# Performance work log

Measured on AMD Instinct MI355X. Metric: run time of the kernel, lower is better.

The kernel has to match this reference:

```python
import math
import jax, jax.numpy as jnp
import numpy as np

N_HEAD = 8


def setup_inputs() -> dict:
    key = jax.random.key(0)
    ks = jax.random.split(key, 9)
    B, S, D = 4, 2048, 512
    s = 1.0 / math.sqrt(D)
    return {
        "x": jax.random.normal(ks[0], (B, S, D), jnp.float32),
        "Wq": jax.random.normal(ks[1], (D, D), jnp.float32) * s,
        "bq": jax.random.normal(ks[2], (D,), jnp.float32) * s,
        "Wk": jax.random.normal(ks[3], (D, D), jnp.float32) * s,
        "bk": jax.random.normal(ks[4], (D,), jnp.float32) * s,
        "Wv": jax.random.normal(ks[5], (D, D), jnp.float32) * s,
        "bv": jax.random.normal(ks[6], (D,), jnp.float32) * s,
        "Wo": jax.random.normal(ks[7], (D, D), jnp.float32) * s,
        "bo": jax.random.normal(ks[8], (D,), jnp.float32) * s,
    }


def reference(x, Wq, bq, Wk, bk, Wv, bv, Wo, bo):
    B, S, D = x.shape
    H = N_HEAD
    hd = D // H
    # projections -> [B, H, S, hd]
    def split_heads(y):
        return y.reshape(B, S, H, hd).transpose(0, 2, 1, 3)
    q = split_heads(x @ Wq + bq)
    k = split_heads(x @ Wk + bk)
    v = split_heads(x @ Wv + bv)
    scale = 1.0 / math.sqrt(hd)
    scores = jnp.einsum("bhqd,bhkd->bhqk", q, k) * scale  # [B,H,S,S]
    attn = jax.nn.softmax(scores, axis=-1)
    ctx = jnp.einsum("bhqk,bhkd->bhqd", attn, v)  # [B,H,S,hd]
    ctx = ctx.transpose(0, 2, 1, 3).reshape(B, S, D)
    out = ctx @ Wo + bo
    avg_attn = attn.mean(axis=1)  # [B,S,S]
    return out, avg_attn
```

## Files before the change

### kernel.cpp

```cpp
#include <hip/hip_runtime.h>

typedef __bf16 bf16;
typedef __bf16 bf16x8 __attribute__((ext_vector_type(8)));
typedef float  f32x4  __attribute__((ext_vector_type(4)));

#define MFMA16(a,b,c) __builtin_amdgcn_mfma_f32_16x16x32_bf16((a),(b),(c),0,0,0)

#define BATCH 4
#define SEQ   2048
#define DIM   512
#define NH    8
#define HD    64
#define QSCALE 0.18033688f

__device__ __forceinline__ bf16x8 ldsfrag(const bf16* t, int row, int kc, int quad){
    int unit = ((kc << 2) + quad) ^ (row & 7);
    return *(const bf16x8*)(t + row * 64 + unit * 8);
}

__device__ __forceinline__ void stage64x64(const bf16* src, long rowStride, bf16* dst, int tid){
#pragma unroll
    for (int rnd = 0; rnd < 2; ++rnd){
        int sid = tid + rnd * 256;
        int row = sid >> 3, s = sid & 7;
        bf16x8 val = *(const bf16x8*)(src + (long)row * rowStride + s * 8);
        *(bf16x8*)(dst + row * 64 + ((s ^ (row & 7)) << 3)) = val;
    }
}

__global__ __launch_bounds__(256) void cvt_x(const float* __restrict__ x, bf16* __restrict__ xb){
    int i = blockIdx.x * 256 + threadIdx.x;
    float4 f = ((const float4*)x)[i];
    bf16* o = xb + 4 * (long)i;
    o[0] = (bf16)f.x; o[1] = (bf16)f.y; o[2] = (bf16)f.z; o[3] = (bf16)f.w;
}

__global__ __launch_bounds__(256) void cvt_wt(const float* __restrict__ Wq, const float* __restrict__ Wk,
                                              const float* __restrict__ Wv, const float* __restrict__ Wo,
                                              bf16* __restrict__ WTb){
    int z = blockIdx.z;
    const float* W = (z == 0) ? Wq : (z == 1) ? Wk : (z == 2) ? Wv : Wo;
    bf16* WT = WTb + (long)z * DIM * DIM;
    __shared__ float lt[32 * 33];
    int t = threadIdx.x, r0 = t >> 5, c = t & 31;
    int k0 = blockIdx.x * 32, n0 = blockIdx.y * 32;
#pragma unroll
    for (int i = 0; i < 4; ++i){
        int row = r0 + i * 8;
        lt[row * 33 + c] = W[(long)(k0 + row) * DIM + n0 + c];
    }
    __syncthreads();
#pragma unroll
    for (int i = 0; i < 4; ++i){
        int nr = r0 + i * 8;
        WT[(long)(n0 + nr) * DIM + k0 + c] = (bf16)lt[c * 33 + nr];
    }
}

__global__ __launch_bounds__(256) void gemm_qkv(const bf16* __restrict__ X, const bf16* __restrict__ WTb,
                                                const float* __restrict__ bq, const float* __restrict__ bk,
                                                const float* __restrict__ bv, bf16* __restrict__ outb){
    __shared__ __align__(16) bf16 lA[128 * 64];
    __shared__ __align__(16) bf16 lB[128 * 64];
    int z = blockIdx.z;
    const bf16* WT = WTb + (long)z * DIM * DIM;
    const float* bias = (z == 0) ? bq : (z == 1) ? bk : bv;
    float qs = (z == 0) ? QSCALE : 1.0f;
    bf16* out = outb + (long)z * BATCH * SEQ * DIM;
    int tid = threadIdx.x, lane = tid & 63, w = tid >> 6;
    int wm = w >> 1, wn = w & 1;
    int m0 = blockIdx.y * 128, n0 = blockIdx.x * 128;
    int r16 = lane & 15, quad = lane >> 4;
    f32x4 zz = {0.f, 0.f, 0.f, 0.f};
    f32x4 acc[4][4];
#pragma unroll
    for (int a = 0; a < 4; ++a)
#pragma unroll
        for (int b2 = 0; b2 < 4; ++b2) acc[a][b2] = zz;

    for (int k0 = 0; k0 < DIM; k0 += 64){
        __syncthreads();
#pragma unroll
        for (int rnd = 0; rnd < 4; ++rnd){
            int sid = tid + rnd * 256;
            int row = sid >> 3, s = sid & 7;
            *(bf16x8*)(lA + row * 64 + ((s ^ (row & 7)) << 3)) =
                *(const bf16x8*)(X + (long)(m0 + row) * DIM + k0 + s * 8);
            *(bf16x8*)(lB + row * 64 + ((s ^ (row & 7)) << 3)) =
                *(const bf16x8*)(WT + (long)(n0 + row) * DIM + k0 + s * 8);
        }
        __syncthreads();
#pragma unroll
        for (int kc = 0; kc < 2; ++kc){
            bf16x8 aF[4], bF[4];
#pragma unroll
            for (int i = 0; i < 4; ++i){
                aF[i] = ldsfrag(lA, wm * 64 + i * 16 + r16, kc, quad);
                bF[i] = ldsfrag(lB, wn * 64 + i * 16 + r16, kc, quad);
            }
#pragma unroll
            for (int rb = 0; rb < 4; ++rb)
#pragma unroll
                for (int nb = 0; nb < 4; ++nb)
                    acc[rb][nb] = MFMA16(aF[rb], bF[nb], acc[rb][nb]);
        }
    }
#pragma unroll
    for (int nb = 0; nb < 4; ++nb){
        int col = n0 + wn * 64 + nb * 16 + r16;
        float bv_ = bias[col];
        int hh = col >> 6, d = col & 63;
#pragma unroll
        for (int rb = 0; rb < 4; ++rb)
#pragma unroll
            for (int r = 0; r < 4; ++r){
                int row = m0 + wm * 64 + rb * 16 + quad * 4 + r;
                int bb = row >> 11, s = row & 2047;
                out[((long)(bb * NH + hh) * SEQ + s) * HD + d] = (bf16)((acc[rb][nb][r] + bv_) * qs);
            }
    }
}

__global__ __launch_bounds__(256) void vtrans(const bf16* __restrict__ v, bf16* __restrict__ vT){
    __shared__ bf16 lt[64 * 72];
    int tid = threadIdx.x;
    int s0 = blockIdx.x * 64;
    int bh = blockIdx.z * NH + blockIdx.y;
#pragma unroll
    for (int rnd = 0; rnd < 2; ++rnd){
        int sid = tid + rnd * 256;
        int row = sid >> 3, sg = sid & 7;
        *(bf16x8*)(lt + row * 72 + sg * 8) =
            *(const bf16x8*)(v + ((long)bh * SEQ + s0 + row) * HD + sg * 8);
    }
    __syncthreads();
#pragma unroll
    for (int rnd = 0; rnd < 2; ++rnd){
        int sid = tid + rnd * 256;
        int d = sid >> 3, sg = sid & 7;
        bf16x8 o;
#pragma unroll
        for (int j = 0; j < 8; ++j) o[j] = lt[(sg * 8 + j) * 72 + d];
        *(bf16x8*)(vT + ((long)bh * HD + d) * SEQ + s0 + sg * 8) = o;
    }
}

__global__ __launch_bounds__(256) void attn_flash(const bf16* __restrict__ q, const bf16* __restrict__ k,
                                                  const bf16* __restrict__ vT, bf16* __restrict__ ctx,
                                                  float* __restrict__ linv_g){
    __shared__ __align__(16) bf16 lQ[64 * 64];
    __shared__ __align__(16) bf16 lK[64 * 64];
    __shared__ __align__(16) bf16 lV[64 * 64];
    __shared__ __align__(16) bf16 lP[4][16 * 64];
    int tid = threadIdx.x, lane = tid & 63, w = tid >> 6;
    int h = blockIdx.y, b = blockIdx.z;
    int bh = b * NH + h;
    int q0 = blockIdx.x * 64;
    int r16 = lane & 15, quad = lane >> 4;

    stage64x64(q + ((long)bh * SEQ + q0) * HD, HD, lQ, tid);
    __syncthreads();
    bf16x8 aF0 = ldsfrag(lQ, w * 16 + r16, 0, quad);
    bf16x8 aF1 = ldsfrag(lQ, w * 16 + r16, 1, quad);

    f32x4 zz = {0.f, 0.f, 0.f, 0.f};
    f32x4 ctxacc[4];
    float lsum[4] = {0.f, 0.f, 0.f, 0.f};
#pragma unroll
    for (int cb = 0; cb < 4; ++cb) ctxacc[cb] = zz;

    for (int j0 = 0; j0 < SEQ; j0 += 64){
        __syncthreads();
        stage64x64(k + ((long)bh * SEQ + j0) * HD, HD, lK, tid);
        stage64x64(vT + (long)bh * HD * SEQ + j0, SEQ, lV, tid);
        __syncthreads();
        __builtin_amdgcn_s_setprio(1);
#pragma unroll
        for (int cb = 0; cb < 4; ++cb){
            f32x4 sa = zz;
            sa = MFMA16(aF0, ldsfrag(lK, cb * 16 + r16, 0, quad), sa);
            sa = MFMA16(aF1, ldsfrag(lK, cb * 16 + r16, 1, quad), sa);
#pragma unroll
            for (int r = 0; r < 4; ++r){
                float p = __builtin_amdgcn_exp2f(sa[r]);
                lsum[r] += p;
                int row = quad * 4 + r, col = cb * 16 + r16;
                int unit = (col >> 3) ^ (row & 7);
                lP[w][row * 64 + unit * 8 + (col & 7)] = (bf16)p;
            }
        }
        asm volatile("s_waitcnt lgkmcnt(0)" ::: "memory");
#pragma unroll
        for (int kc = 0; kc < 2; ++kc){
            bf16x8 pF = ldsfrag(lP[w], r16, kc, quad);
#pragma unroll
            for (int cb = 0; cb < 4; ++cb)
                ctxacc[cb] = MFMA16(pF, ldsfrag(lV, cb * 16 + r16, kc, quad), ctxacc[cb]);
        }
        __builtin_amdgcn_s_setprio(0);
    }
#pragma unroll
    for (int m = 1; m < 16; m <<= 1)
#pragma unroll
        for (int r = 0; r < 4; ++r) lsum[r] += __shfl_xor(lsum[r], m, 64);
    float rinv[4];
#pragma unroll
    for (int r = 0; r < 4; ++r) rinv[r] = 1.0f / lsum[r];
#pragma unroll
    for (int cb = 0; cb < 4; ++cb)
#pragma unroll
        for (int r = 0; r < 4; ++r){
            long srow = q0 + w * 16 + quad * 4 + r;
            ctx[((long)b * SEQ + srow) * DIM + h * HD + cb * 16 + r16] = (bf16)(ctxacc[cb][r] * rinv[r]);
        }
    if (r16 == 0)
#pragma unroll
        for (int r = 0; r < 4; ++r)
            linv_g[(long)bh * SEQ + q0 + w * 16 + quad * 4 + r] = rinv[r];
}

__global__ __launch_bounds__(256) void attn_avg(const bf16* __restrict__ q, const bf16* __restrict__ k,
                                                const float* __restrict__ linv_g, float* __restrict__ avg){
    int lin  = blockIdx.x + (blockIdx.y << 3) + (blockIdx.z << 8);
    int task = ((lin & 7) << 7) + (lin >> 3);
    int qb_ = task & 7;
    int jt  = (task >> 3) & 31;
    int b   = task >> 8;
    int tid = threadIdx.x, lane = tid & 63, w = tid >> 6;
    int r16 = lane & 15, quad = lane >> 4;
    int qbase = qb_ * 256 + w * 64;
    int j0 = jt * 64;

    f32x4 zz = {0.f, 0.f, 0.f, 0.f};
    f32x4 psum[4][4];
#pragma unroll
    for (int rb = 0; rb < 4; ++rb)
#pragma unroll
        for (int cb = 0; cb < 4; ++cb) psum[rb][cb] = zz;

#pragma unroll 1
    for (int hh = 0; hh < NH; ++hh){
        long hA = (long)b * NH + hh;
        const bf16*  qh = q + (hA * SEQ + qbase) * HD;
        const bf16*  kh = k + (hA * SEQ + j0) * HD;
        const float* lh = linv_g + hA * SEQ + qbase;

        bf16x8 aF[4][2];
        float4 lvv[4];
#pragma unroll
        for (int rb = 0; rb < 4; ++rb){
            aF[rb][0] = *(const bf16x8*)(qh + (rb * 16 + r16) * HD + quad * 8);
            aF[rb][1] = *(const bf16x8*)(qh + (rb * 16 + r16) * HD + 32 + quad * 8);
            lvv[rb]   = *(const float4*)(lh + rb * 16 + quad * 4);
        }
#pragma unroll
        for (int cb = 0; cb < 4; ++cb){
            bf16x8 bF0 = *(const bf16x8*)(kh + (cb * 16 + r16) * HD + quad * 8);
            bf16x8 bF1 = *(const bf16x8*)(kh + (cb * 16 + r16) * HD + 32 + quad * 8);
#pragma unroll
            for (int rb = 0; rb < 4; ++rb){
                f32x4 sa = MFMA16(aF[rb][0], bF0, zz);
                sa = MFMA16(aF[rb][1], bF1, sa);
#pragma unroll
                for (int r = 0; r < 4; ++r)
                    psum[rb][cb][r] += __builtin_amdgcn_exp2f(sa[r]) * lvv[rb][r];
            }
        }
    }
#pragma unroll
    for (int rb = 0; rb < 4; ++rb)
#pragma unroll
        for (int cb = 0; cb < 4; ++cb)
#pragma unroll
            for (int r = 0; r < 4; ++r){
                long row = qbase + rb * 16 + quad * 4 + r;
                __builtin_nontemporal_store(psum[rb][cb][r] * 0.125f,
                    &avg[((long)b * SEQ + row) * SEQ + j0 + cb * 16 + r16]);
            }
}

__global__ __launch_bounds__(256) void gemm_out(const bf16* __restrict__ CTX, const bf16* __restrict__ WT,
                                                const float* __restrict__ bo, float* __restrict__ out){
    __shared__ __align__(16) bf16 lA[128 * 64];
    __shared__ __align__(16) bf16 lB[128 * 64];
    int tid = threadIdx.x, lane = tid & 63, w = tid >> 6;
    int wm = w >> 1, wn = w & 1;
    int m0 = blockIdx.y * 128, n0 = blockIdx.x * 128;
    int r16 = lane & 15, quad = lane >> 4;
    f32x4 zz = {0.f, 0.f, 0.f, 0.f};
    f32x4 acc[4][4];
#pragma unroll
    for (int a = 0; a < 4; ++a)
#pragma unroll
        for (int b2 = 0; b2 < 4; ++b2) acc[a][b2] = zz;

    for (int k0 = 0; k0 < DIM; k0 += 64){
        __syncthreads();
#pragma unroll
        for (int rnd = 0; rnd < 4; ++rnd){
            int sid = tid + rnd * 256;
            int row = sid >> 3, s = sid & 7;
            *(bf16x8*)(lA + row * 64 + ((s ^ (row & 7)) << 3)) =
                *(const bf16x8*)(CTX + (long)(m0 + row) * DIM + k0 + s * 8);
            *(bf16x8*)(lB + row * 64 + ((s ^ (row & 7)) << 3)) =
                *(const bf16x8*)(WT + (long)(n0 + row) * DIM + k0 + s * 8);
        }
        __syncthreads();
#pragma unroll
        for (int kc = 0; kc < 2; ++kc){
            bf16x8 aF[4], bF[4];
#pragma unroll
            for (int i = 0; i < 4; ++i){
                aF[i] = ldsfrag(lA, wm * 64 + i * 16 + r16, kc, quad);
                bF[i] = ldsfrag(lB, wn * 64 + i * 16 + r16, kc, quad);
            }
#pragma unroll
            for (int rb2 = 0; rb2 < 4; ++rb2)
#pragma unroll
                for (int nb = 0; nb < 4; ++nb)
                    acc[rb2][nb] = MFMA16(aF[rb2], bF[nb], acc[rb2][nb]);
        }
    }
#pragma unroll
    for (int nb = 0; nb < 4; ++nb){
        int col = n0 + wn * 64 + nb * 16 + r16;
        float bv_ = bo[col];
#pragma unroll
        for (int rb2 = 0; rb2 < 4; ++rb2)
#pragma unroll
            for (int r = 0; r < 4; ++r){
                int row = m0 + wm * 64 + rb2 * 16 + quad * 4 + r;
                out[(long)row * DIM + col] = acc[rb2][nb][r] + bv_;
            }
    }
}

extern "C" void kernel_launch(void* const* d_in, const int* in_sizes, int n_in,
                              void* d_out, int out_size, void* d_ws, size_t ws_size,
                              hipStream_t stream) {
    const float* x  = (const float*)d_in[0];
    const float* Wq = (const float*)d_in[1];
    const float* bq = (const float*)d_in[2];
    const float* Wk = (const float*)d_in[3];
    const float* bk = (const float*)d_in[4];
    const float* Wv = (const float*)d_in[5];
    const float* bv = (const float*)d_in[6];
    const float* Wo = (const float*)d_in[7];
    const float* bo = (const float*)d_in[8];
    float* out = (float*)d_out;

    char* ws = (char*)d_ws;
    bf16*  xb   = (bf16*)(ws);
    bf16*  WT   = (bf16*)(ws + 8388608);
    bf16*  qb   = (bf16*)(ws + 10485760);
    bf16*  kb   = qb + (long)BATCH * SEQ * DIM;
    bf16*  vb   = kb + (long)BATCH * SEQ * DIM;
    bf16*  vT   = (bf16*)(ws + 35651584);
    bf16*  ctx  = (bf16*)(ws + 44040192);
    float* linv = (float*)(ws + 52428800);

    cvt_x    <<<4096, 256, 0, stream>>>(x, xb);
    cvt_wt   <<<dim3(16, 16, 4), 256, 0, stream>>>(Wq, Wk, Wv, Wo, WT);
    gemm_qkv <<<dim3(4, 64, 3), 256, 0, stream>>>(xb, WT, bq, bk, bv, qb);
    vtrans   <<<dim3(32, 8, 4), 256, 0, stream>>>(vb, vT);
    attn_flash<<<dim3(32, 8, 4), 256, 0, stream>>>(qb, kb, vT, ctx, linv);
    attn_avg <<<dim3(8, 32, 4), 256, 0, stream>>>(qb, kb, linv, out + (long)BATCH * SEQ * DIM);
    gemm_out <<<dim3(4, 64), 256, 0, stream>>>(ctx, WT + 3L * DIM * DIM, bo, out);
}
```

Measured before the change: 286.9 us.

## Prefetch K/V tiles into registers in flash loop and shrink attn_avg tiles

The flash-attention loop now loads the next K and V^T tile into registers before computing the current tile, then writes them to LDS after a barrier. This hides global-load latency behind the MFMA work. The attn_avg kernel is changed to 32 query rows per wave instead of 64, which doubles the grid, and its stores are reordered per row. The trade-off is more register pressure in the flash kernel and, in attn_avg, more redundant K loads across the larger grid.

```diff
diff --git a/kernel.cpp b/kernel.cpp
--- a/kernel.cpp
+++ b/kernel.cpp
@@ -169,11 +169,25 @@
 #pragma unroll
     for (int cb = 0; cb < 4; ++cb) ctxacc[cb] = zz;
 
-    for (int j0 = 0; j0 < SEQ; j0 += 64){
-        __syncthreads();
-        stage64x64(k + ((long)bh * SEQ + j0) * HD, HD, lK, tid);
-        stage64x64(vT + (long)bh * HD * SEQ + j0, SEQ, lV, tid);
-        __syncthreads();
+    int r0_ = tid >> 3, s_ = tid & 7;
+    const bf16* kbase = k + (long)bh * SEQ * HD;
+    const bf16* vbase = vT + (long)bh * HD * SEQ;
+    bf16x8 kr0, kr1, vr0, vr1;
+
+    auto LOADREGS = [&](int j0){
+        kr0 = *(const bf16x8*)(kbase + (long)(j0 + r0_) * HD + s_ * 8);
+        kr1 = *(const bf16x8*)(kbase + (long)(j0 + r0_ + 32) * HD + s_ * 8);
+        vr0 = *(const bf16x8*)(vbase + (long)r0_ * SEQ + j0 + s_ * 8);
+        vr1 = *(const bf16x8*)(vbase + (long)(r0_ + 32) * SEQ + j0 + s_ * 8);
+    };
+    auto WRITELDS = [&](){
+        int u = (s_ ^ (r0_ & 7)) << 3;
+        *(bf16x8*)(lK + r0_ * 64 + u) = kr0;
+        *(bf16x8*)(lK + (r0_ + 32) * 64 + u) = kr1;
+        *(bf16x8*)(lV + r0_ * 64 + u) = vr0;
+        *(bf16x8*)(lV + (r0_ + 32) * 64 + u) = vr1;
+    };
+    auto COMPUTE = [&](){
         __builtin_amdgcn_s_setprio(1);
 #pragma unroll
         for (int cb = 0; cb < 4; ++cb){
@@ -190,6 +204,7 @@
             }
         }
         asm volatile("s_waitcnt lgkmcnt(0)" ::: "memory");
+        __builtin_amdgcn_sched_barrier(0);
 #pragma unroll
         for (int kc = 0; kc < 2; ++kc){
             bf16x8 pF = ldsfrag(lP[w], r16, kc, quad);
@@ -198,7 +213,20 @@
                 ctxacc[cb] = MFMA16(pF, ldsfrag(lV, cb * 16 + r16, kc, quad), ctxacc[cb]);
         }
         __builtin_amdgcn_s_setprio(0);
-    }
+    };
+
+    LOADREGS(0);
+    WRITELDS();
+    __syncthreads();
+    for (int j0 = 0; j0 < SEQ - 64; j0 += 64){
+        LOADREGS(j0 + 64);
+        COMPUTE();
+        __syncthreads();
+        WRITELDS();
+        __syncthreads();
+    }
+    COMPUTE();
+
 #pragma unroll
     for (int m = 1; m < 16; m <<= 1)
 #pragma unroll
@@ -221,20 +249,20 @@
 
 __global__ __launch_bounds__(256) void attn_avg(const bf16* __restrict__ q, const bf16* __restrict__ k,
                                                 const float* __restrict__ linv_g, float* __restrict__ avg){
-    int lin  = blockIdx.x + (blockIdx.y << 3) + (blockIdx.z << 8);
-    int task = ((lin & 7) << 7) + (lin >> 3);
-    int qb_ = task & 7;
-    int jt  = (task >> 3) & 31;
-    int b   = task >> 8;
+    int lin  = blockIdx.x + (blockIdx.y << 4) + (blockIdx.z << 9);
+    int task = ((lin & 7) << 8) + (lin >> 3);
+    int qt  = task & 15;
+    int jt  = (task >> 4) & 31;
+    int b   = task >> 9;
     int tid = threadIdx.x, lane = tid & 63, w = tid >> 6;
     int r16 = lane & 15, quad = lane >> 4;
-    int qbase = qb_ * 256 + w * 64;
+    int qbase = qt * 128 + w * 32;
     int j0 = jt * 64;
 
     f32x4 zz = {0.f, 0.f, 0.f, 0.f};
-    f32x4 psum[4][4];
-#pragma unroll
-    for (int rb = 0; rb < 4; ++rb)
+    f32x4 psum[2][4];
+#pragma unroll
+    for (int rb = 0; rb < 2; ++rb)
 #pragma unroll
         for (int cb = 0; cb < 4; ++cb) psum[rb][cb] = zz;
 
@@ -245,10 +273,10 @@
         const bf16*  kh = k + (hA * SEQ + j0) * HD;
         const float* lh = linv_g + hA * SEQ + qbase;
 
-        bf16x8 aF[4][2];
-        float4 lvv[4];
-#pragma unroll
-        for (int rb = 0; rb < 4; ++rb){
+        bf16x8 aF[2][2];
+        float4 lvv[2];
+#pragma unroll
+        for (int rb = 0; rb < 2; ++rb){
             aF[rb][0] = *(const bf16x8*)(qh + (rb * 16 + r16) * HD + quad * 8);
             aF[rb][1] = *(const bf16x8*)(qh + (rb * 16 + r16) * HD + 32 + quad * 8);
             lvv[rb]   = *(const float4*)(lh + rb * 16 + quad * 4);
@@ -258,7 +286,7 @@
             bf16x8 bF0 = *(const bf16x8*)(kh + (cb * 16 + r16) * HD + quad * 8);
             bf16x8 bF1 = *(const bf16x8*)(kh + (cb * 16 + r16) * HD + 32 + quad * 8);
 #pragma unroll
-            for (int rb = 0; rb < 4; ++rb){
+            for (int rb = 0; rb < 2; ++rb){
                 f32x4 sa = MFMA16(aF[rb][0], bF0, zz);
                 sa = MFMA16(aF[rb][1], bF1, sa);
 #pragma unroll
@@ -268,15 +296,15 @@
         }
     }
 #pragma unroll
-    for (int rb = 0; rb < 4; ++rb)
-#pragma unroll
-        for (int cb = 0; cb < 4; ++cb)
-#pragma unroll
-            for (int r = 0; r < 4; ++r){
-                long row = qbase + rb * 16 + quad * 4 + r;
-                __builtin_nontemporal_store(psum[rb][cb][r] * 0.125f,
-                    &avg[((long)b * SEQ + row) * SEQ + j0 + cb * 16 + r16]);
-            }
+    for (int rb = 0; rb < 2; ++rb)
+#pragma unroll
+        for (int r = 0; r < 4; ++r){
+            long row = qbase + rb * 16 + quad * 4 + r;
+            float* dst = avg + ((long)b * SEQ + row) * SEQ + j0 + r16;
+#pragma unroll
+            for (int cb = 0; cb < 4; ++cb)
+                __builtin_nontemporal_store(psum[rb][cb][r] * 0.125f, dst + cb * 16);
+        }
 }
 
 __global__ __launch_bounds__(256) void gemm_out(const bf16* __restrict__ CTX, const bf16* __restrict__ WT,
@@ -364,6 +392,6 @@
     gemm_qkv <<<dim3(4, 64, 3), 256, 0, stream>>>(xb, WT, bq, bk, bv, qb);
     vtrans   <<<dim3(32, 8, 4), 256, 0, stream>>>(vb, vT);
     attn_flash<<<dim3(32, 8, 4), 256, 0, stream>>>(qb, kb, vT, ctx, linv);
-    attn_avg <<<dim3(8, 32, 4), 256, 0, stream>>>(qb, kb, linv, out + (long)BATCH * SEQ * DIM);
+    attn_avg <<<dim3(16, 32, 4), 256, 0, stream>>>(qb, kb, linv, out + (long)BATCH * SEQ * DIM);
     gemm_out <<<dim3(4, 64), 256, 0, stream>>>(ctx, WT + 3L * DIM * DIM, bo, out);
 }
```

Measured after the change: 308.2 us. 1.07x slower.
